# Optimization experiments

Hardware: AMD Instinct MI355X
Metric: run time of the kernel (lower is better)

## Reference

```python
import jax, jax.numpy as jnp
import numpy as np

# TT decomposition config (from Eff_TTEmbedding args in source)
P = (216, 216, 216)      # auto-factorized p_shapes for n=10,000,000 (216^3 >= n)
Q = (2, 4, 2)            # tt_q_shapes, prod = 16 = embedding_dim
R = (128, 128)           # tt_ranks
NUM_TABLES = 2
BATCH = 1024
NUM_EMB = 10_000_000


def setup_inputs() -> dict:
    key = jax.random.key(0)
    k0, k1, k2, k3 = jax.random.split(key, 4)
    # sparse indices per TT table: [n_tables, batch]
    lS_i = jax.random.randint(k3, (NUM_TABLES, BATCH), 0, NUM_EMB, dtype=jnp.int64)
    # TT cores, weight_dist='uniform'
    core0 = jax.random.uniform(k0, (NUM_TABLES, P[0], Q[0] * R[0]), dtype=jnp.float32, minval=-0.01, maxval=0.01)
    core1 = jax.random.uniform(k1, (NUM_TABLES, P[1], R[0] * Q[1] * R[1]), dtype=jnp.float32, minval=-0.01, maxval=0.01)
    core2 = jax.random.uniform(k2, (NUM_TABLES, P[2], R[1] * Q[2]), dtype=jnp.float32, minval=-0.01, maxval=0.01)
    return {"lS_i": lS_i, "core0": core0, "core1": core1, "core2": core2}


def _tt_lookup(idx, c0, c1, c2):
    """TT embedding lookup for one table. idx: [B] int; returns [B, prod(Q)]."""
    B = idx.shape[0]
    # mixed-radix decomposition of flat index into (i0, i1, i2)
    i0 = idx // (P[1] * P[2])
    i1 = (idx // P[2]) % P[1]
    i2 = idx % P[2]
    # gather TT core slices (the memory-bound irregular access)
    A = c0[i0].reshape(B, Q[0], R[0])            # [B, 2, 128]
    Bm = c1[i1].reshape(B, R[0], Q[1] * R[1])    # [B, 128, 512]
    C = c2[i2].reshape(B, R[1], Q[2])            # [B, 128, 2]
    # chained small matmuls along TT ranks
    AB = jnp.einsum('bqr,brs->bqs', A, Bm).reshape(B, Q[0] * Q[1], R[1])  # [B, 8, 128]
    out = jnp.einsum('bqr,brs->bqs', AB, C)      # [B, 8, 2]
    return out.reshape(B, Q[0] * Q[1] * Q[2])    # [B, 16]


def reference(lS_i, core0, core1, core2):
    # per-table dispatch (forward returns one embedding bag per TT table)
    return jax.vmap(_tt_lookup)(lS_i, core0, core1, core2)  # [n_tables, B, 16]
```

## Files before the change

### kernel.cpp

```cpp
#include <hip/hip_runtime.h>


#define CAP  48
#define CAPP 52

__global__ __launch_bounds__(64) void tt_fused(
    const int* __restrict__ idx32,
    const float* __restrict__ c0,
    const float* __restrict__ c1,
    const float* __restrict__ c2,
    float* __restrict__ out)
{
    const int g     = blockIdx.x;
    const int qh    = blockIdx.y;
    const int lh    = blockIdx.z;
    const int table = g / 216;
    const int i1    = g - table * 216;
    const int tl    = threadIdx.x;

    __shared__ float lds[1024];
    __shared__ int s_id[CAPP];
    __shared__ int s_aux[CAPP];

    if (tl < CAPP) s_aux[tl] = 0;

    const bool is64 = (idx32[1] == 0) & (idx32[3] == 0) &
                      (idx32[5] == 0) & (idx32[7] == 0);

    unsigned v[16];
    if (is64) {
        const long long* p = (const long long*)idx32 + (table << 10) + tl;
#pragma unroll
        for (int it = 0; it < 16; ++it) v[it] = (unsigned)p[it * 64];
    } else {
        const int* p = idx32 + (table << 10) + tl;
#pragma unroll
        for (int it = 0; it < 16; ++it) v[it] = (unsigned)p[it * 64];
    }
    int cnt = 0;
#pragma unroll
    for (int it = 0; it < 16; ++it) {
        const unsigned idx = v[it];
        const unsigned i0  = idx / 46656u;
        const unsigned rem = idx - i0 * 46656u;
        const unsigned bi1 = rem / 216u;
        const bool match = ((int)bi1 == i1);
        const unsigned long long mask = __ballot(match);
        if (match) {
            const int pos = cnt + __popcll(mask & ((1ull << tl) - 1ull));
            if (pos < CAP) {
                const unsigned i2 = rem - bi1 * 216u;
                s_id[pos]  = (table << 10) + it * 64 + tl;
                s_aux[pos] = (int)((i0 << 16) | i2);
            }
        }
        cnt += (int)__popcll(mask);
    }
    const int m = min(cnt, CAP);
    if (m <= lh * 4) return;

    float2*       lds2 = (float2*)lds;
    const float4* lds4 = (const float4*)lds;

    const float4* b4  = (const float4*)(c1 + ((size_t)g << 16) + qh * 256) + tl;
    const float*  c0t = c0 + (size_t)table * 216 * 256;

#define LOADB(BUF, T)                                                       \
    { _Pragma("unroll")                                                     \
      for (int i = 0; i < 4; ++i) BUF[i] = b4[(size_t)((T) * 4 + i) * 128]; }

#define FMAB(BUF, T)                                                        \
    { _Pragma("unroll")                                                     \
      for (int l = 0; l < 4; ++l) {                                         \
        _Pragma("unroll")                                                   \
        for (int j = 0; j < 2; ++j) {                                       \
          const float4 av = lds4[l * 64 + (T) * 2 + j];                     \
          const float4 b0 = BUF[2 * j], b1 = BUF[2 * j + 1];                \
          acc0[l].x += av.x * b0.x; acc0[l].y += av.x * b0.y;               \
          acc0[l].z += av.x * b0.z; acc0[l].w += av.x * b0.w;               \
          acc0[l].x += av.z * b1.x; acc0[l].y += av.z * b1.y;               \
          acc0[l].z += av.z * b1.z; acc0[l].w += av.z * b1.w;               \
          acc1[l].x += av.y * b0.x; acc1[l].y += av.y * b0.y;               \
          acc1[l].z += av.y * b0.z; acc1[l].w += av.y * b0.w;               \
          acc1[l].x += av.w * b1.x; acc1[l].y += av.w * b1.y;               \
          acc1[l].z += av.w * b1.z; acc1[l].w += av.w * b1.w;               \
        } } }

    for (int base = lh * 4; base < m; base += 8) {
        const int cl = min(4, m - base);

#pragma unroll
        for (int l = 0; l < 4; ++l) {
            const float* ar = c0t + (size_t)(s_aux[base + l] >> 16) * 256;
            const float x0 = ar[tl],       x1 = ar[tl + 64];
            const float y0 = ar[tl + 128], y1 = ar[tl + 192];
            lds2[l * 128 + tl]      = make_float2(x0, y0);
            lds2[l * 128 + tl + 64] = make_float2(x1, y1);
        }

        float4 acc0[4], acc1[4];
#pragma unroll
        for (int l = 0; l < 4; ++l) {
            acc0[l] = make_float4(0.f, 0.f, 0.f, 0.f);
            acc1[l] = make_float4(0.f, 0.f, 0.f, 0.f);
        }

        float4 bufA[4], bufB[4];
        LOADB(bufA, 0)
        for (int T = 0; T < 30; T += 2) {
            LOADB(bufB, T + 1)
            FMAB(bufA, T)
            LOADB(bufA, T + 2)
            FMAB(bufB, T + 1)
        }
        LOADB(bufB, 31)
        FMAB(bufA, 30)
        FMAB(bufB, 31)

        const int half = tl >> 5;
        const int r1b  = (tl & 31) * 4;
#pragma unroll
        for (int l = 0; l < 4; ++l) {
            if (l < cl) {
                const float* crow =
                    c2 + (size_t)(table * 216 + (s_aux[base + l] & 0xffff)) * 256;
                const float4 cv0 = *(const float4*)(crow + r1b * 2);
                const float4 cv1 = *(const float4*)(crow + r1b * 2 + 4);
                float p00 = acc0[l].x * cv0.x + acc0[l].y * cv0.z
                          + acc0[l].z * cv1.x + acc0[l].w * cv1.z;
                float p01 = acc0[l].x * cv0.y + acc0[l].y * cv0.w
                          + acc0[l].z * cv1.y + acc0[l].w * cv1.w;
                float p10 = acc1[l].x * cv0.x + acc1[l].y * cv0.z
                          + acc1[l].z * cv1.x + acc1[l].w * cv1.z;
                float p11 = acc1[l].x * cv0.y + acc1[l].y * cv0.w
                          + acc1[l].z * cv1.y + acc1[l].w * cv1.w;
#pragma unroll
                for (int mm = 16; mm >= 1; mm >>= 1) {
                    p00 += __shfl_xor(p00, mm);
                    p01 += __shfl_xor(p01, mm);
                    p10 += __shfl_xor(p10, mm);
                    p11 += __shfl_xor(p11, mm);
                }
                if ((tl & 31) == 0) {
                    float* o = out + (size_t)s_id[base + l] * 16;
                    const int q1 = qh * 2 + half;
                    *(float2*)(o + q1 * 2)     = make_float2(p00, p01);
                    *(float2*)(o + 8 + q1 * 2) = make_float2(p10, p11);
                }
            }
        }
    }
#undef LOADB
#undef FMAB
}

extern "C" void kernel_launch(void* const* d_in, const int* in_sizes, int n_in,
                              void* d_out, int out_size, void* d_ws, size_t ws_size,
                              hipStream_t stream) {
    const int*   idx = (const int*)d_in[0];
    const float* c0  = (const float*)d_in[1];
    const float* c1  = (const float*)d_in[2];
    const float* c2  = (const float*)d_in[3];
    float* out = (float*)d_out;
    (void)d_ws; (void)ws_size; (void)in_sizes; (void)n_in; (void)out_size;

    tt_fused<<<dim3(432, 2, 2), dim3(64), 0, stream>>>(idx, c0, c1, c2, out);
}
```

Measured before the change: 183.1 us.

## Split rank reduction across two waves and process eight lookups per block

The launch drops the z-split over lookup groups and uses 128-thread blocks in which two wavefronts each take half of the 128-wide rank dimension, processing eight lookups per pass. Partial accumulators are reduced through shared memory before the core2 contraction. The first c1 tile load is issued before the index scan so it overlaps the bucketing work. Each c1 slice is now read once per block instead of by two separate blocks, at the cost of extra barriers, higher register pressure from eight accumulator pairs, and an idle wave during the epilogue.

```diff
diff --git a/kernel.cpp b/kernel.cpp
--- a/kernel.cpp
+++ b/kernel.cpp
@@ -2,9 +2,9 @@
 
 
 #define CAP  48
-#define CAPP 52
+#define CAPP 56
 
-__global__ __launch_bounds__(64) void tt_fused(
+__global__ __launch_bounds__(128) void tt_fused(
     const int* __restrict__ idx32,
     const float* __restrict__ c0,
     const float* __restrict__ c1,
@@ -13,16 +13,50 @@
 {
     const int g     = blockIdx.x;
     const int qh    = blockIdx.y;
-    const int lh    = blockIdx.z;
     const int table = g / 216;
     const int i1    = g - table * 216;
-    const int tl    = threadIdx.x;
 
-    __shared__ float lds[1024];
+    const int tid = threadIdx.x;
+    const int rh  = tid >> 6;
+    const int tl  = tid & 63;
+
+    __shared__ float lds[4096];
     __shared__ int s_id[CAPP];
     __shared__ int s_aux[CAPP];
 
-    if (tl < CAPP) s_aux[tl] = 0;
+    if (tid < CAPP) s_aux[tid] = 0;
+
+    float2*       lds2 = (float2*)lds;
+    float4*       lds4w = (float4*)lds;
+    const float4* lds4 = (const float4*)lds;
+
+    const float4* b4  = (const float4*)(c1 + ((size_t)g << 16) + qh * 256) + tl;
+    const float*  c0t = c0 + (size_t)table * 216 * 256;
+
+#define LOADB(BUF, T)                                                       \
+    { _Pragma("unroll")                                                     \
+      for (int i = 0; i < 4; ++i)                                           \
+          BUF[i] = b4[(size_t)(rh * 64 + (T) * 4 + i) * 128]; }
+
+#define FMAB(BUF, T)                                                        \
+    { _Pragma("unroll")                                                     \
+      for (int l = 0; l < 8; ++l) {                                         \
+        _Pragma("unroll")                                                   \
+        for (int j = 0; j < 2; ++j) {                                       \
+          const float4 av = lds4[l * 64 + rh * 32 + (T) * 2 + j];           \
+          const float4 b0 = BUF[2 * j], b1 = BUF[2 * j + 1];                \
+          acc0[l].x += av.x * b0.x; acc0[l].y += av.x * b0.y;               \
+          acc0[l].z += av.x * b0.z; acc0[l].w += av.x * b0.w;               \
+          acc0[l].x += av.z * b1.x; acc0[l].y += av.z * b1.y;               \
+          acc0[l].z += av.z * b1.z; acc0[l].w += av.z * b1.w;               \
+          acc1[l].x += av.y * b0.x; acc1[l].y += av.y * b0.y;               \
+          acc1[l].z += av.y * b0.z; acc1[l].w += av.y * b0.w;               \
+          acc1[l].x += av.w * b1.x; acc1[l].y += av.w * b1.y;               \
+          acc1[l].z += av.w * b1.z; acc1[l].w += av.w * b1.w;               \
+        } } }
+
+    float4 bufA[4], bufB[4];
+    LOADB(bufA, 0)
 
     const bool is64 = (idx32[1] == 0) & (idx32[3] == 0) &
                       (idx32[5] == 0) & (idx32[7] == 0);
@@ -57,95 +91,89 @@
         cnt += (int)__popcll(mask);
     }
     const int m = min(cnt, CAP);
-    if (m <= lh * 4) return;
+    if (m == 0) return;
 
-    float2*       lds2 = (float2*)lds;
-    const float4* lds4 = (const float4*)lds;
+    for (int base = 0; base < m; base += 8) {
+        const int cl = min(8, m - base);
+        __syncthreads();
 
-    const float4* b4  = (const float4*)(c1 + ((size_t)g << 16) + qh * 256) + tl;
-    const float*  c0t = c0 + (size_t)table * 216 * 256;
+        float a0[8], a1[8];
+#pragma unroll
+        for (int l = 0; l < 8; ++l) {
+            const float* ar = c0t + (size_t)(s_aux[base + l] >> 16) * 256;
+            a0[l] = ar[tid];
+            a1[l] = ar[tid + 128];
+        }
+#pragma unroll
+        for (int l = 0; l < 8; ++l)
+            lds2[l * 128 + tid] = make_float2(a0[l], a1[l]);
+        __syncthreads();
 
-#define LOADB(BUF, T)                                                       \
-    { _Pragma("unroll")                                                     \
-      for (int i = 0; i < 4; ++i) BUF[i] = b4[(size_t)((T) * 4 + i) * 128]; }
-
-#define FMAB(BUF, T)                                                        \
-    { _Pragma("unroll")                                                     \
-      for (int l = 0; l < 4; ++l) {                                         \
-        _Pragma("unroll")                                                   \
-        for (int j = 0; j < 2; ++j) {                                       \
-          const float4 av = lds4[l * 64 + (T) * 2 + j];                     \
-          const float4 b0 = BUF[2 * j], b1 = BUF[2 * j + 1];                \
-          acc0[l].x += av.x * b0.x; acc0[l].y += av.x * b0.y;               \
-          acc0[l].z += av.x * b0.z; acc0[l].w += av.x * b0.w;               \
-          acc0[l].x += av.z * b1.x; acc0[l].y += av.z * b1.y;               \
-          acc0[l].z += av.z * b1.z; acc0[l].w += av.z * b1.w;               \
-          acc1[l].x += av.y * b0.x; acc1[l].y += av.y * b0.y;               \
-          acc1[l].z += av.y * b0.z; acc1[l].w += av.y * b0.w;               \
-          acc1[l].x += av.w * b1.x; acc1[l].y += av.w * b1.y;               \
-          acc1[l].z += av.w * b1.z; acc1[l].w += av.w * b1.w;               \
-        } } }
-
-    for (int base = lh * 4; base < m; base += 8) {
-        const int cl = min(4, m - base);
-
+        float4 acc0[8], acc1[8];
 #pragma unroll
-        for (int l = 0; l < 4; ++l) {
-            const float* ar = c0t + (size_t)(s_aux[base + l] >> 16) * 256;
-            const float x0 = ar[tl],       x1 = ar[tl + 64];
-            const float y0 = ar[tl + 128], y1 = ar[tl + 192];
-            lds2[l * 128 + tl]      = make_float2(x0, y0);
-            lds2[l * 128 + tl + 64] = make_float2(x1, y1);
-        }
-
-        float4 acc0[4], acc1[4];
-#pragma unroll
-        for (int l = 0; l < 4; ++l) {
+        for (int l = 0; l < 8; ++l) {
             acc0[l] = make_float4(0.f, 0.f, 0.f, 0.f);
             acc1[l] = make_float4(0.f, 0.f, 0.f, 0.f);
         }
 
-        float4 bufA[4], bufB[4];
-        LOADB(bufA, 0)
-        for (int T = 0; T < 30; T += 2) {
+        for (int T = 0; T < 14; T += 2) {
             LOADB(bufB, T + 1)
             FMAB(bufA, T)
             LOADB(bufA, T + 2)
             FMAB(bufB, T + 1)
         }
-        LOADB(bufB, 31)
-        FMAB(bufA, 30)
-        FMAB(bufB, 31)
+        LOADB(bufB, 15)
+        FMAB(bufA, 14)
+        FMAB(bufB, 15)
+        if (base + 8 < m) LOADB(bufA, 0)
 
-        const int half = tl >> 5;
-        const int r1b  = (tl & 31) * 4;
+        __syncthreads();
+        if (rh == 1) {
 #pragma unroll
-        for (int l = 0; l < 4; ++l) {
-            if (l < cl) {
-                const float* crow =
-                    c2 + (size_t)(table * 216 + (s_aux[base + l] & 0xffff)) * 256;
-                const float4 cv0 = *(const float4*)(crow + r1b * 2);
-                const float4 cv1 = *(const float4*)(crow + r1b * 2 + 4);
-                float p00 = acc0[l].x * cv0.x + acc0[l].y * cv0.z
-                          + acc0[l].z * cv1.x + acc0[l].w * cv1.z;
-                float p01 = acc0[l].x * cv0.y + acc0[l].y * cv0.w
-                          + acc0[l].z * cv1.y + acc0[l].w * cv1.w;
-                float p10 = acc1[l].x * cv0.x + acc1[l].y * cv0.z
-                          + acc1[l].z * cv1.x + acc1[l].w * cv1.z;
-                float p11 = acc1[l].x * cv0.y + acc1[l].y * cv0.w
-                          + acc1[l].z * cv1.y + acc1[l].w * cv1.w;
+            for (int l = 0; l < 8; ++l) {
+                lds4w[(l * 2 + 0) * 64 + tl] = acc0[l];
+                lds4w[(l * 2 + 1) * 64 + tl] = acc1[l];
+            }
+        }
+        __syncthreads();
+
+        if (rh == 0) {
+            const int half = tl >> 5;
+            const int r1b  = (tl & 31) * 4;
 #pragma unroll
-                for (int mm = 16; mm >= 1; mm >>= 1) {
-                    p00 += __shfl_xor(p00, mm);
-                    p01 += __shfl_xor(p01, mm);
-                    p10 += __shfl_xor(p10, mm);
-                    p11 += __shfl_xor(p11, mm);
-                }
-                if ((tl & 31) == 0) {
-                    float* o = out + (size_t)s_id[base + l] * 16;
-                    const int q1 = qh * 2 + half;
-                    *(float2*)(o + q1 * 2)     = make_float2(p00, p01);
-                    *(float2*)(o + 8 + q1 * 2) = make_float2(p10, p11);
+            for (int l = 0; l < 8; ++l) {
+                const float4 w0 = lds4[(l * 2 + 0) * 64 + tl];
+                const float4 w1 = lds4[(l * 2 + 1) * 64 + tl];
+                const float4 s0 = make_float4(acc0[l].x + w0.x, acc0[l].y + w0.y,
+                                              acc0[l].z + w0.z, acc0[l].w + w0.w);
+                const float4 s1 = make_float4(acc1[l].x + w1.x, acc1[l].y + w1.y,
+                                              acc1[l].z + w1.z, acc1[l].w + w1.w);
+                if (l < cl) {
+                    const float* crow =
+                        c2 + (size_t)(table * 216 + (s_aux[base + l] & 0xffff)) * 256;
+                    const float4 cv0 = *(const float4*)(crow + r1b * 2);
+                    const float4 cv1 = *(const float4*)(crow + r1b * 2 + 4);
+                    float p00 = s0.x * cv0.x + s0.y * cv0.z
+                              + s0.z * cv1.x + s0.w * cv1.z;
+                    float p01 = s0.x * cv0.y + s0.y * cv0.w
+                              + s0.z * cv1.y + s0.w * cv1.w;
+                    float p10 = s1.x * cv0.x + s1.y * cv0.z
+                              + s1.z * cv1.x + s1.w * cv1.z;
+                    float p11 = s1.x * cv0.y + s1.y * cv0.w
+                              + s1.z * cv1.y + s1.w * cv1.w;
+#pragma unroll
+                    for (int mm = 16; mm >= 1; mm >>= 1) {
+                        p00 += __shfl_xor(p00, mm);
+                        p01 += __shfl_xor(p01, mm);
+                        p10 += __shfl_xor(p10, mm);
+                        p11 += __shfl_xor(p11, mm);
+                    }
+                    if ((tl & 31) == 0) {
+                        float* o = out + (size_t)s_id[base + l] * 16;
+                        const int q1 = qh * 2 + half;
+                        *(float2*)(o + q1 * 2)     = make_float2(p00, p01);
+                        *(float2*)(o + 8 + q1 * 2) = make_float2(p10, p11);
+                    }
                 }
             }
         }
@@ -164,5 +192,5 @@
     float* out = (float*)d_out;
     (void)d_ws; (void)ws_size; (void)in_sizes; (void)n_in; (void)out_size;
 
-    tt_fused<<<dim3(432, 2, 2), dim3(64), 0, stream>>>(idx, c0, c1, c2, out);
+    tt_fused<<<dim3(432, 2), dim3(128), 0, stream>>>(idx, c0, c1, c2, out);
 }
```

After: 190.4 us. 4.0% more time.
